# Performance work log

Measured on AMD Instinct MI355X. Metric: run time of the kernel, lower is better.

The kernel has to match this reference:

```python
import jax, jax.numpy as jnp
import numpy as np

B, S, D, H = 8, 2048, 1024, 64


def setup_inputs() -> dict:
    key = jax.random.key(0)
    ks = jax.random.split(key, 9)
    s = 0.02
    return {
        "x": jax.random.normal(ks[0], (B, S, D), jnp.float32),
        "Wq": jax.random.normal(ks[1], (H, D), jnp.float32) * s,
        "bq": jnp.zeros((H,), jnp.float32),
        "Wk": jax.random.normal(ks[2], (H, D), jnp.float32) * s,
        "bk": jnp.zeros((H,), jnp.float32),
        "Wv": jax.random.normal(ks[3], (H, D), jnp.float32) * s,
        "bv": jnp.zeros((H,), jnp.float32),
        "Wo": jax.random.normal(ks[4], (H, H), jnp.float32) * s,
        "bo": jnp.zeros((H,), jnp.float32),
    }


def reference(x, Wq, bq, Wk, bk, Wv, bv, Wo, bo):
    # Linear layers: y = x @ W.T + b (torch nn.Linear convention)
    q = jnp.einsum("bsd,hd->bsh", x, Wq) + bq  # [B,S,H]
    k = jnp.einsum("bsd,hd->bsh", x, Wk) + bk
    v = jnp.einsum("bsd,hd->bsh", x, Wv) + bv
    scale = jnp.float32(H) ** 0.5
    scores = jnp.einsum("bsh,bth->bst", q, k) / scale  # [B,S,S]
    causal = jnp.tril(jnp.ones((S, S), bool))
    scores = jnp.where(causal, scores, -jnp.inf)
    attn = jax.nn.softmax(scores, axis=-1)
    out = jnp.einsum("bst,bth->bsh", attn, v)  # [B,S,H]
    out = jnp.einsum("bsh,gh->bsg", out, Wo) + bo  # output proj [H,H]
    return out
```

## Files before the change

kernel.cpp:

```cpp
#include <hip/hip_runtime.h>
#include <hip/hip_bf16.h>

#define NB 8
#define NS 2048
#define ND 1024
#define NH 64
#define NM (NB*NS)

typedef __attribute__((ext_vector_type(8))) short short8;
typedef __attribute__((ext_vector_type(4))) short short4v;
typedef __attribute__((ext_vector_type(4))) float f32x4;
typedef __attribute__((ext_vector_type(4))) float f4;

#define QSCALE (0.125f * 1.44269504088896340736f)

__device__ __forceinline__ unsigned short f2bf(float f) {
    union { __hip_bfloat16 h; unsigned short u; } cv;
    cv.h = __float2bfloat16(f);
    return cv.u;
}

__global__ __launch_bounds__(256) void convw_kernel(
    const float* __restrict__ Wq, const float* __restrict__ bq,
    const float* __restrict__ Wk, const float* __restrict__ bk,
    const float* __restrict__ Wv, const float* __restrict__ bv,
    const float* __restrict__ Wo,
    unsigned short* __restrict__ Wb, unsigned short* __restrict__ Wob,
    float* __restrict__ biasb)
{
    const int row = blockIdx.x;
    const int t = threadIdx.x;
    if (row < 192) {
        const float* W = row < 64 ? Wq : (row < 128 ? Wk : Wv);
        const float sc = row < 64 ? QSCALE : 1.0f;
        f4 v = *(const f4*)&W[(size_t)(row & 63) * ND + t * 4];
        short4v o;
#pragma unroll
        for (int j = 0; j < 4; ++j) o[j] = (short)f2bf(v[j] * sc);
        *(short4v*)&Wb[(size_t)row * ND + t * 4] = o;
        if (row == 0 && t < 192) {
            const float* bsrc = t < 64 ? bq : (t < 128 ? bk : bv);
            biasb[t] = bsrc[t & 63] * (t < 64 ? QSCALE : 1.0f);
        }
    } else if (t < 16) {
        f4 v = *(const f4*)&Wo[(size_t)(row - 192) * 64 + t * 4];
        short4v o;
#pragma unroll
        for (int j = 0; j < 4; ++j) o[j] = (short)f2bf(v[j]);
        *(short4v*)&Wob[(size_t)(row - 192) * 64 + t * 4] = o;
    }
}

__global__ __launch_bounds__(512) void qkv_kernel(
    const float* __restrict__ x, const unsigned short* __restrict__ Wb,
    const float* __restrict__ biasb,
    unsigned short* __restrict__ q, unsigned short* __restrict__ k,
    unsigned short* __restrict__ vT)
{
    __shared__ unsigned short As[2][64 * 64];
    __shared__ unsigned short Bs[2][192 * 64];

    const int t = threadIdx.x;
    const int lane = t & 63, g = lane >> 4, li = lane & 15;
    const int w = t >> 6, rg = w >> 2, cg = w & 3;
    const int m0 = blockIdx.x * 64;
    const int arow = t >> 3, ach = t & 7;

    f32x4 acc[2][3];
#pragma unroll
    for (int a = 0; a < 2; ++a)
#pragma unroll
        for (int nf = 0; nf < 3; ++nf) acc[a][nf] = (f32x4)0.f;

    f4 xa[2][2]; short8 wr[2][3];

#define QKV_LOAD(KS, SL)                                                          \
    {                                                                             \
        const float* p_ = &x[(size_t)(m0 + arow) * ND + (KS) * 64 + ach * 8];     \
        xa[SL][0] = *(const f4*)p_; xa[SL][1] = *(const f4*)(p_ + 4);             \
        wr[SL][0] = *(const short8*)&Wb[(size_t)(t >> 3) * ND + (KS) * 64 + (t & 7) * 8];                  \
        wr[SL][1] = *(const short8*)&Wb[(size_t)((t + 512) >> 3) * ND + (KS) * 64 + ((t + 512) & 7) * 8];  \
        wr[SL][2] = *(const short8*)&Wb[(size_t)((t + 1024) >> 3) * ND + (KS) * 64 + ((t + 1024) & 7) * 8];\
    }

#define QKV_COMMIT(SL, BUF)                                                       \
    {                                                                             \
        short8 av_;                                                               \
        for (int j_ = 0; j_ < 4; ++j_) {                                          \
            av_[j_] = (short)f2bf(xa[SL][0][j_]);                                 \
            av_[j_ + 4] = (short)f2bf(xa[SL][1][j_]);                             \
        }                                                                         \
        *(short8*)&As[BUF][arow * 64 + ((ach ^ (arow & 7)) << 3)] = av_;          \
        int r0_ = t >> 3, c0_ = t & 7;                                            \
        *(short8*)&Bs[BUF][r0_ * 64 + ((c0_ ^ (r0_ & 7)) << 3)] = wr[SL][0];      \
        int r1_ = (t + 512) >> 3, c1_ = (t + 512) & 7;                            \
        *(short8*)&Bs[BUF][r1_ * 64 + ((c1_ ^ (r1_ & 7)) << 3)] = wr[SL][1];      \
        int r2_ = (t + 1024) >> 3, c2_ = (t + 1024) & 7;                          \
        *(short8*)&Bs[BUF][r2_ * 64 + ((c2_ ^ (r2_ & 7)) << 3)] = wr[SL][2];      \
    }

    QKV_LOAD(0, 0);
    QKV_LOAD(1, 1);
    QKV_COMMIT(0, 0);
    __syncthreads();

#pragma unroll
    for (int ks = 0; ks < 16; ++ks) {
        const int cur = ks & 1;
        if (ks < 14) QKV_LOAD(ks + 2, cur);
#pragma unroll
        for (int h = 0; h < 2; ++h) {
            short8 af0 = *(const short8*)&As[cur][(rg * 32 + 0 + li) * 64 + (((g + 4 * h) ^ (li & 7)) << 3)];
            short8 af1 = *(const short8*)&As[cur][(rg * 32 + 16 + li) * 64 + (((g + 4 * h) ^ (li & 7)) << 3)];
#pragma unroll
            for (int nf = 0; nf < 3; ++nf) {
                short8 bf = *(const short8*)&Bs[cur][(cg * 48 + nf * 16 + li) * 64 + (((g + 4 * h) ^ (li & 7)) << 3)];
                acc[0][nf] = __builtin_amdgcn_mfma_f32_16x16x32_bf16(af0, bf, acc[0][nf], 0, 0, 0);
                acc[1][nf] = __builtin_amdgcn_mfma_f32_16x16x32_bf16(af1, bf, acc[1][nf], 0, 0, 0);
            }
        }
        if (ks < 15) QKV_COMMIT((ks + 1) & 1, cur ^ 1);
        __syncthreads();
    }

#pragma unroll
    for (int nf = 0; nf < 3; ++nf) {
        const int col = cg * 48 + nf * 16 + li;
        const float bias = biasb[col];
#pragma unroll
        for (int a = 0; a < 2; ++a) {
            const int row0 = m0 + rg * 32 + a * 16 + 4 * g;
            if (col < 64) {
#pragma unroll
                for (int i = 0; i < 4; ++i)
                    q[(size_t)(row0 + i) * NH + col] = f2bf(acc[a][nf][i] + bias);
            } else if (col < 128) {
#pragma unroll
                for (int i = 0; i < 4; ++i)
                    k[(size_t)(row0 + i) * NH + (col - 64)] = f2bf(acc[a][nf][i] + bias);
            } else {
                short4v pk;
#pragma unroll
                for (int i = 0; i < 4; ++i) pk[i] = (short)f2bf(acc[a][nf][i] + bias);
                const int bb = row0 >> 11, s = row0 & 2047;
                *(short4v*)&vT[(size_t)(bb * NH + (col - 128)) * NS + s] = pk;
            }
        }
    }
}

__global__ __launch_bounds__(256) void attn_kernel(
    const unsigned short* __restrict__ q, const unsigned short* __restrict__ k,
    const unsigned short* __restrict__ vT,
    float* __restrict__ Opart, float* __restrict__ lpart,
    int ctLog, int MAXC)
{
    __shared__ unsigned short Ks[2][64 * 64];
    __shared__ unsigned short Vs[2][64 * 64];
    __shared__ unsigned short Ps[4][16 * 64];

    const int t = threadIdx.x;
    const int w = t >> 6, lane = t & 63, g = lane >> 4, li = lane & 15;
    const int b = blockIdx.x & 7;
    const int pid = blockIdx.x >> 3;
    const int CT = 1 << ctLog;

    int qt = 0, c = 0;
    {
        int acc = 0;
        for (int u = 31; u >= 0; --u) {
            int nch = (u + CT) >> ctLog;
            if (pid < acc + nch) { qt = u; c = pid - acc; break; }
            acc += nch;
        }
    }
    const int t0 = c * CT;
    const int rem = qt + 1 - t0;
    const int tcount = rem < CT ? rem : CT;

    const size_t qkbase = (size_t)b * NS * NH;
    const int qrow = qt * 64 + w * 16 + li;
    const short8 qa0 = *(const short8*)&q[qkbase + (size_t)qrow * NH + g * 8];
    const short8 qa1 = *(const short8*)&q[qkbase + (size_t)qrow * NH + 32 + g * 8];

    float l_i[4]; f32x4 oacc[4];
#pragma unroll
    for (int i = 0; i < 4; ++i) { l_i[i] = 0.f; oacc[i] = (f32x4)0.f; }

    const int srow = t >> 3, sch = t & 7;
    short8 kreg0, kreg1, vreg0, vreg1;

    {
        const int kv0 = t0 * 64;
        kreg0 = *(const short8*)&k[qkbase + (size_t)(kv0 + srow) * NH + sch * 8];
        kreg1 = *(const short8*)&k[qkbase + (size_t)(kv0 + srow + 32) * NH + sch * 8];
        vreg0 = *(const short8*)&vT[(size_t)(b * NH + srow) * NS + kv0 + sch * 8];
        vreg1 = *(const short8*)&vT[(size_t)(b * NH + srow + 32) * NS + kv0 + sch * 8];
        *(short8*)&Ks[0][srow * 64 + ((sch ^ (srow & 7)) << 3)] = kreg0;
        *(short8*)&Ks[0][(srow + 32) * 64 + ((sch ^ (srow & 7)) << 3)] = kreg1;
        *(short8*)&Vs[0][srow * 64 + ((sch ^ (srow & 7)) << 3)] = vreg0;
        *(short8*)&Vs[0][(srow + 32) * 64 + ((sch ^ (srow & 7)) << 3)] = vreg1;
    }
    __syncthreads();

    for (int tt = 0; tt < tcount; ++tt) {
        const int cur = tt & 1;
        const int kv0 = (t0 + tt) * 64;
        if (tt + 1 < tcount) {
            const int nv0 = kv0 + 64;
            kreg0 = *(const short8*)&k[qkbase + (size_t)(nv0 + srow) * NH + sch * 8];
            kreg1 = *(const short8*)&k[qkbase + (size_t)(nv0 + srow + 32) * NH + sch * 8];
            vreg0 = *(const short8*)&vT[(size_t)(b * NH + srow) * NS + nv0 + sch * 8];
            vreg1 = *(const short8*)&vT[(size_t)(b * NH + srow + 32) * NS + nv0 + sch * 8];
        }
        f32x4 s[4];
#pragma unroll
        for (int c4 = 0; c4 < 4; ++c4) {
            s[c4] = (f32x4)0.f;
            const int krow = 16 * c4 + li;
            short8 kf0 = *(const short8*)&Ks[cur][krow * 64 + ((g ^ (li & 7)) << 3)];
            s[c4] = __builtin_amdgcn_mfma_f32_16x16x32_bf16(qa0, kf0, s[c4], 0, 0, 0);
            short8 kf1 = *(const short8*)&Ks[cur][krow * 64 + (((g + 4) ^ (li & 7)) << 3)];
            s[c4] = __builtin_amdgcn_mfma_f32_16x16x32_bf16(qa1, kf1, s[c4], 0, 0, 0);
        }
        if (kv0 == qt * 64) {
#pragma unroll
            for (int c4 = 0; c4 < 4; ++c4)
#pragma unroll
                for (int i = 0; i < 4; ++i)
                    if (16 * c4 + li > w * 16 + 4 * g + i) s[c4][i] = -1e30f;
        }
        float p[4][4];
#pragma unroll
        for (int c4 = 0; c4 < 4; ++c4)
#pragma unroll
            for (int i = 0; i < 4; ++i)
                p[c4][i] = exp2f(fminf(s[c4][i], 80.f));
#pragma unroll
        for (int i = 0; i < 4; ++i)
            l_i[i] += (p[0][i] + p[1][i]) + (p[2][i] + p[3][i]);

#pragma unroll
        for (int c4 = 0; c4 < 4; ++c4)
#pragma unroll
            for (int i = 0; i < 4; ++i) {
                const int prow = 4 * g + i;
                const int chunk = 2 * c4 + (li >> 3);
                Ps[w][prow * 64 + ((chunk ^ (prow & 7)) << 3) + (li & 7)] = f2bf(p[c4][i]);
            }
        short8 pf0 = *(const short8*)&Ps[w][li * 64 + ((g ^ (li & 7)) << 3)];
        short8 pf1 = *(const short8*)&Ps[w][li * 64 + (((g + 4) ^ (li & 7)) << 3)];
#pragma unroll
        for (int nf = 0; nf < 4; ++nf) {
            const int vrow = nf * 16 + li;
            short8 vf0 = *(const short8*)&Vs[cur][vrow * 64 + ((g ^ (li & 7)) << 3)];
            short8 vf1 = *(const short8*)&Vs[cur][vrow * 64 + (((g + 4) ^ (li & 7)) << 3)];
            oacc[nf] = __builtin_amdgcn_mfma_f32_16x16x32_bf16(pf0, vf0, oacc[nf], 0, 0, 0);
            oacc[nf] = __builtin_amdgcn_mfma_f32_16x16x32_bf16(pf1, vf1, oacc[nf], 0, 0, 0);
        }
        if (tt + 1 < tcount) {
            *(short8*)&Ks[cur ^ 1][srow * 64 + ((sch ^ (srow & 7)) << 3)] = kreg0;
            *(short8*)&Ks[cur ^ 1][(srow + 32) * 64 + ((sch ^ (srow & 7)) << 3)] = kreg1;
            *(short8*)&Vs[cur ^ 1][srow * 64 + ((sch ^ (srow & 7)) << 3)] = vreg0;
            *(short8*)&Vs[cur ^ 1][(srow + 32) * 64 + ((sch ^ (srow & 7)) << 3)] = vreg1;
        }
        __syncthreads();
    }

#pragma unroll
    for (int off = 1; off < 16; off <<= 1)
#pragma unroll
        for (int i = 0; i < 4; ++i) l_i[i] += __shfl_xor(l_i[i], off);

    const size_t slot = (size_t)((b * 32 + qt) * MAXC + c);
    float* Op = Opart + slot * 4096;
#pragma unroll
    for (int nf = 0; nf < 4; ++nf)
#pragma unroll
        for (int i = 0; i < 4; ++i)
            Op[(w * 16 + 4 * g + i) * 64 + nf * 16 + li] = oacc[nf][i];
    if (li == 0) {
#pragma unroll
        for (int i = 0; i < 4; ++i)
            lpart[slot * 64 + w * 16 + 4 * g + i] = l_i[i];
    }
}

__global__ __launch_bounds__(256) void combine_kernel(
    const float* __restrict__ Opart, const float* __restrict__ lpart,
    const unsigned short* __restrict__ Wob, const float* __restrict__ bo,
    float* __restrict__ out, int ctLog, int MAXC)
{
    __shared__ unsigned short Osm[64 * 64];
    __shared__ float Linv[64];

    const int t = threadIdx.x;
    const int b = blockIdx.x & 7, qt = blockIdx.x >> 3;
    const int CT = 1 << ctLog;
    const int nch = (qt + CT) >> ctLog;
    const size_t base_slot = (size_t)(b * 32 + qt) * MAXC;

    if (t < 64) {
        float L = 0.f;
        for (int cc = 0; cc < nch; ++cc)
            L += lpart[(base_slot + cc) * 64 + t];
        Linv[t] = 1.f / L;
    }

    const int r = t >> 2, c0 = (t & 3) * 16;
    f4 a0 = (f4)0.f, a1 = (f4)0.f, a2 = (f4)0.f, a3 = (f4)0.f;
    for (int cc = 0; cc < nch; ++cc) {
        const float* P = Opart + (base_slot + cc) * 4096 + r * 64 + c0;
        a0 += *(const f4*)P; a1 += *(const f4*)(P + 4);
        a2 += *(const f4*)(P + 8); a3 += *(const f4*)(P + 12);
    }
    __syncthreads();
    {
        const float sc = Linv[r];
        short8 o0, o1;
#pragma unroll
        for (int j = 0; j < 4; ++j) {
            o0[j] = (short)f2bf(a0[j] * sc); o0[j + 4] = (short)f2bf(a1[j] * sc);
            o1[j] = (short)f2bf(a2[j] * sc); o1[j + 4] = (short)f2bf(a3[j] * sc);
        }
        const int ch0 = (t & 3) * 2;
        *(short8*)&Osm[r * 64 + ((ch0 ^ (r & 7)) << 3)] = o0;
        *(short8*)&Osm[r * 64 + (((ch0 + 1) ^ (r & 7)) << 3)] = o1;
    }
    __syncthreads();

    const int w = t >> 6, lane = t & 63, g = lane >> 4, li = lane & 15;
    f32x4 acc[4];
#pragma unroll
    for (int nf = 0; nf < 4; ++nf) acc[nf] = (f32x4)0.f;
#pragma unroll
    for (int s = 0; s < 2; ++s) {
        short8 af = *(const short8*)&Osm[(w * 16 + li) * 64 + (((g + 4 * s) ^ (li & 7)) << 3)];
#pragma unroll
        for (int nf = 0; nf < 4; ++nf) {
            short8 bf = *(const short8*)&Wob[(size_t)(nf * 16 + li) * 64 + s * 32 + g * 8];
            acc[nf] = __builtin_amdgcn_mfma_f32_16x16x32_bf16(af, bf, acc[nf], 0, 0, 0);
        }
    }
#pragma unroll
    for (int nf = 0; nf < 4; ++nf) {
        const float bias = bo[nf * 16 + li];
#pragma unroll
        for (int i = 0; i < 4; ++i) {
            const size_t row = (size_t)b * NS + qt * 64 + w * 16 + 4 * g + i;
            out[row * 64 + nf * 16 + li] = acc[nf][i] + bias;
        }
    }
}

extern "C" void kernel_launch(void* const* d_in, const int* in_sizes, int n_in,
                              void* d_out, int out_size, void* d_ws, size_t ws_size,
                              hipStream_t stream)
{
    const float* x  = (const float*)d_in[0];
    const float* Wq = (const float*)d_in[1];
    const float* bq = (const float*)d_in[2];
    const float* Wk = (const float*)d_in[3];
    const float* bk = (const float*)d_in[4];
    const float* Wv = (const float*)d_in[5];
    const float* bv = (const float*)d_in[6];
    const float* Wo = (const float*)d_in[7];
    const float* bo = (const float*)d_in[8];
    float* out = (float*)d_out;

    size_t off = 0;
    auto alloc = [&](size_t bytes) {
        char* p = (char*)d_ws + off;
        off += (bytes + 255) & ~(size_t)255;
        return (void*)p;
    };
    unsigned short* qb  = (unsigned short*)alloc((size_t)NM * NH * 2);
    unsigned short* kb  = (unsigned short*)alloc((size_t)NM * NH * 2);
    unsigned short* vtb = (unsigned short*)alloc((size_t)NM * NH * 2);
    unsigned short* Wb  = (unsigned short*)alloc((size_t)192 * ND * 2);
    unsigned short* Wob = (unsigned short*)alloc((size_t)64 * 64 * 2);
    float* biasb = (float*)alloc(192 * 4);
    const size_t base = off;

    int ctLog = 5, MAXC = 1;
    const int cands[3] = {3, 4, 5};
    for (int ci = 0; ci < 3; ++ci) {
        const int cl = cands[ci];
        const int mc = (31 >> cl) + 1;
        const size_t nslot = (size_t)256 * mc;
        const size_t need = base + nslot * (4096 + 64) * 4 + 8192;
        if (need <= ws_size) { ctLog = cl; MAXC = mc; break; }
    }
    const size_t NSLOT = (size_t)256 * MAXC;
    float* Opart = (float*)alloc(NSLOT * 4096 * 4);
    float* lpart = (float*)alloc(NSLOT * 64 * 4);

    const int CT = 1 << ctLog;
    int NCperB = 0;
    for (int qt = 0; qt < 32; ++qt) NCperB += (qt + CT) >> ctLog;

    convw_kernel<<<256, 256, 0, stream>>>(Wq, bq, Wk, bk, Wv, bv, Wo, Wb, Wob, biasb);
    qkv_kernel<<<NM / 64, 512, 0, stream>>>(x, Wb, biasb, qb, kb, vtb);
    attn_kernel<<<8 * NCperB, 256, 0, stream>>>(qb, kb, vtb, Opart, lpart, ctLog, MAXC);
    combine_kernel<<<256, 256, 0, stream>>>(Opart, lpart, Wob, bo, out, ctLog, MAXC);
}
```

Baseline: 50.21 us.

## Load weights and K/V fragments directly from global into registers, enlarge query tiles

The QKV projection now reads weight fragments straight from global memory into registers with double buffering, dropping the shared-memory B tile and its stores. The attention kernel now processes 128-query blocks, 32 rows per wave, and has each wave load its K and V MFMA fragments directly from global memory with no shared staging or block barriers. Each wave also exits early past the causal boundary. The combine kernel and the workspace slot layout are adjusted to match. This cuts LDS traffic and barrier stalls but adds redundant global/L2 reads across waves and more register pressure.

```diff
diff --git a/kernel.cpp b/kernel.cpp
--- a/kernel.cpp
+++ b/kernel.cpp
@@ -58,7 +58,6 @@
     unsigned short* __restrict__ vT)
 {
     __shared__ unsigned short As[2][64 * 64];
-    __shared__ unsigned short Bs[2][192 * 64];
 
     const int t = threadIdx.x;
     const int lane = t & 63, g = lane >> 4, li = lane & 15;
@@ -72,54 +71,59 @@
 #pragma unroll
         for (int nf = 0; nf < 3; ++nf) acc[a][nf] = (f32x4)0.f;
 
-    f4 xa[2][2]; short8 wr[2][3];
-
-#define QKV_LOAD(KS, SL)                                                          \
-    {                                                                             \
-        const float* p_ = &x[(size_t)(m0 + arow) * ND + (KS) * 64 + ach * 8];     \
-        xa[SL][0] = *(const f4*)p_; xa[SL][1] = *(const f4*)(p_ + 4);             \
-        wr[SL][0] = *(const short8*)&Wb[(size_t)(t >> 3) * ND + (KS) * 64 + (t & 7) * 8];                  \
-        wr[SL][1] = *(const short8*)&Wb[(size_t)((t + 512) >> 3) * ND + (KS) * 64 + ((t + 512) & 7) * 8];  \
-        wr[SL][2] = *(const short8*)&Wb[(size_t)((t + 1024) >> 3) * ND + (KS) * 64 + ((t + 1024) & 7) * 8];\
-    }
-
-#define QKV_COMMIT(SL, BUF)                                                       \
-    {                                                                             \
-        short8 av_;                                                               \
-        for (int j_ = 0; j_ < 4; ++j_) {                                          \
-            av_[j_] = (short)f2bf(xa[SL][0][j_]);                                 \
-            av_[j_ + 4] = (short)f2bf(xa[SL][1][j_]);                             \
-        }                                                                         \
-        *(short8*)&As[BUF][arow * 64 + ((ach ^ (arow & 7)) << 3)] = av_;          \
-        int r0_ = t >> 3, c0_ = t & 7;                                            \
-        *(short8*)&Bs[BUF][r0_ * 64 + ((c0_ ^ (r0_ & 7)) << 3)] = wr[SL][0];      \
-        int r1_ = (t + 512) >> 3, c1_ = (t + 512) & 7;                            \
-        *(short8*)&Bs[BUF][r1_ * 64 + ((c1_ ^ (r1_ & 7)) << 3)] = wr[SL][1];      \
-        int r2_ = (t + 1024) >> 3, c2_ = (t + 1024) & 7;                          \
-        *(short8*)&Bs[BUF][r2_ * 64 + ((c2_ ^ (r2_ & 7)) << 3)] = wr[SL][2];      \
-    }
-
-    QKV_LOAD(0, 0);
-    QKV_LOAD(1, 1);
-    QKV_COMMIT(0, 0);
+    f4 xa[2][2];
+    short8 bfr[2][3][2];
+
+#define XLOAD(KS, SL)                                                         \
+    {                                                                         \
+        const float* p_ = &x[(size_t)(m0 + arow) * ND + (KS) * 64 + ach * 8]; \
+        xa[SL][0] = *(const f4*)p_; xa[SL][1] = *(const f4*)(p_ + 4);         \
+    }
+
+#define XCOMMIT(SL, BUF)                                                      \
+    {                                                                         \
+        short8 av_;                                                           \
+        for (int j_ = 0; j_ < 4; ++j_) {                                      \
+            av_[j_] = (short)f2bf(xa[SL][0][j_]);                             \
+            av_[j_ + 4] = (short)f2bf(xa[SL][1][j_]);                         \
+        }                                                                     \
+        *(short8*)&As[BUF][arow * 64 + ((ach ^ (arow & 7)) << 3)] = av_;      \
+    }
+
+#define WLOAD(KS, SL)                                                         \
+    {                                                                         \
+        _Pragma("unroll")                                                     \
+        for (int nf_ = 0; nf_ < 3; ++nf_)                                     \
+            _Pragma("unroll")                                                 \
+            for (int h_ = 0; h_ < 2; ++h_)                                    \
+                bfr[SL][nf_][h_] = *(const short8*)&Wb[                       \
+                    (size_t)(cg * 48 + nf_ * 16 + li) * ND + (KS) * 64 +      \
+                    h_ * 32 + g * 8];                                         \
+    }
+
+    XLOAD(0, 0);
+    XLOAD(1, 1);
+    WLOAD(0, 0);
+    XCOMMIT(0, 0);
     __syncthreads();
 
 #pragma unroll
     for (int ks = 0; ks < 16; ++ks) {
         const int cur = ks & 1;
-        if (ks < 14) QKV_LOAD(ks + 2, cur);
+        const int wb = ks & 1;
+        if (ks < 15) WLOAD(ks + 1, wb ^ 1);
+        if (ks < 14) XLOAD(ks + 2, cur);
 #pragma unroll
         for (int h = 0; h < 2; ++h) {
             short8 af0 = *(const short8*)&As[cur][(rg * 32 + 0 + li) * 64 + (((g + 4 * h) ^ (li & 7)) << 3)];
             short8 af1 = *(const short8*)&As[cur][(rg * 32 + 16 + li) * 64 + (((g + 4 * h) ^ (li & 7)) << 3)];
 #pragma unroll
             for (int nf = 0; nf < 3; ++nf) {
-                short8 bf = *(const short8*)&Bs[cur][(cg * 48 + nf * 16 + li) * 64 + (((g + 4 * h) ^ (li & 7)) << 3)];
-                acc[0][nf] = __builtin_amdgcn_mfma_f32_16x16x32_bf16(af0, bf, acc[0][nf], 0, 0, 0);
-                acc[1][nf] = __builtin_amdgcn_mfma_f32_16x16x32_bf16(af1, bf, acc[1][nf], 0, 0, 0);
+                acc[0][nf] = __builtin_amdgcn_mfma_f32_16x16x32_bf16(af0, bfr[wb][nf][h], acc[0][nf], 0, 0, 0);
+                acc[1][nf] = __builtin_amdgcn_mfma_f32_16x16x32_bf16(af1, bfr[wb][nf][h], acc[1][nf], 0, 0, 0);
             }
         }
-        if (ks < 15) QKV_COMMIT((ks + 1) & 1, cur ^ 1);
+        if (ks < 15) XCOMMIT((ks + 1) & 1, cur ^ 1);
         __syncthreads();
     }
 
@@ -155,9 +159,7 @@
     float* __restrict__ Opart, float* __restrict__ lpart,
     int ctLog, int MAXC)
 {
-    __shared__ unsigned short Ks[2][64 * 64];
-    __shared__ unsigned short Vs[2][64 * 64];
-    __shared__ unsigned short Ps[4][16 * 64];
+    __shared__ unsigned short Ps[4][32 * 64];
 
     const int t = threadIdx.x;
     const int w = t >> 6, lane = t & 63, g = lane >> 4, li = lane & 15;
@@ -165,124 +167,137 @@
     const int pid = blockIdx.x >> 3;
     const int CT = 1 << ctLog;
 
-    int qt = 0, c = 0;
+    int qb = 0, c = 0;
     {
         int acc = 0;
-        for (int u = 31; u >= 0; --u) {
-            int nch = (u + CT) >> ctLog;
-            if (pid < acc + nch) { qt = u; c = pid - acc; break; }
+        for (int u = 15; u >= 0; --u) {
+            const int nch = (2 * u + 2 + CT - 1) >> ctLog;
+            if (pid < acc + nch) { qb = u; c = pid - acc; break; }
             acc += nch;
         }
     }
     const int t0 = c * CT;
-    const int rem = qt + 1 - t0;
+    const int ntt = 2 * qb + 2;
+    const int rem = ntt - t0;
     const int tcount = rem < CT ? rem : CT;
 
     const size_t qkbase = (size_t)b * NS * NH;
-    const int qrow = qt * 64 + w * 16 + li;
-    const short8 qa0 = *(const short8*)&q[qkbase + (size_t)qrow * NH + g * 8];
-    const short8 qa1 = *(const short8*)&q[qkbase + (size_t)qrow * NH + 32 + g * 8];
-
-    float l_i[4]; f32x4 oacc[4];
-#pragma unroll
-    for (int i = 0; i < 4; ++i) { l_i[i] = 0.f; oacc[i] = (f32x4)0.f; }
-
-    const int srow = t >> 3, sch = t & 7;
-    short8 kreg0, kreg1, vreg0, vreg1;
-
-    {
-        const int kv0 = t0 * 64;
-        kreg0 = *(const short8*)&k[qkbase + (size_t)(kv0 + srow) * NH + sch * 8];
-        kreg1 = *(const short8*)&k[qkbase + (size_t)(kv0 + srow + 32) * NH + sch * 8];
-        vreg0 = *(const short8*)&vT[(size_t)(b * NH + srow) * NS + kv0 + sch * 8];
-        vreg1 = *(const short8*)&vT[(size_t)(b * NH + srow + 32) * NS + kv0 + sch * 8];
-        *(short8*)&Ks[0][srow * 64 + ((sch ^ (srow & 7)) << 3)] = kreg0;
-        *(short8*)&Ks[0][(srow + 32) * 64 + ((sch ^ (srow & 7)) << 3)] = kreg1;
-        *(short8*)&Vs[0][srow * 64 + ((sch ^ (srow & 7)) << 3)] = vreg0;
-        *(short8*)&Vs[0][(srow + 32) * 64 + ((sch ^ (srow & 7)) << 3)] = vreg1;
-    }
-    __syncthreads();
+    const int q0 = qb * 128 + w * 32;
+    const int qmax = q0 + 31;
+
+    short8 qa[2][2];
+#pragma unroll
+    for (int qs = 0; qs < 2; ++qs)
+#pragma unroll
+        for (int h = 0; h < 2; ++h)
+            qa[qs][h] = *(const short8*)&q[qkbase + (size_t)(q0 + qs * 16 + li) * NH + h * 32 + g * 8];
+
+    float l_i[2][4];
+    f32x4 oacc[2][4];
+#pragma unroll
+    for (int qs = 0; qs < 2; ++qs)
+#pragma unroll
+        for (int i = 0; i < 4; ++i) { l_i[qs][i] = 0.f; oacc[qs][i] = (f32x4)0.f; }
 
     for (int tt = 0; tt < tcount; ++tt) {
-        const int cur = tt & 1;
         const int kv0 = (t0 + tt) * 64;
-        if (tt + 1 < tcount) {
-            const int nv0 = kv0 + 64;
-            kreg0 = *(const short8*)&k[qkbase + (size_t)(nv0 + srow) * NH + sch * 8];
-            kreg1 = *(const short8*)&k[qkbase + (size_t)(nv0 + srow + 32) * NH + sch * 8];
-            vreg0 = *(const short8*)&vT[(size_t)(b * NH + srow) * NS + nv0 + sch * 8];
-            vreg1 = *(const short8*)&vT[(size_t)(b * NH + srow + 32) * NS + nv0 + sch * 8];
-        }
-        f32x4 s[4];
-#pragma unroll
-        for (int c4 = 0; c4 < 4; ++c4) {
-            s[c4] = (f32x4)0.f;
-            const int krow = 16 * c4 + li;
-            short8 kf0 = *(const short8*)&Ks[cur][krow * 64 + ((g ^ (li & 7)) << 3)];
-            s[c4] = __builtin_amdgcn_mfma_f32_16x16x32_bf16(qa0, kf0, s[c4], 0, 0, 0);
-            short8 kf1 = *(const short8*)&Ks[cur][krow * 64 + (((g + 4) ^ (li & 7)) << 3)];
-            s[c4] = __builtin_amdgcn_mfma_f32_16x16x32_bf16(qa1, kf1, s[c4], 0, 0, 0);
-        }
-        if (kv0 == qt * 64) {
+        if (kv0 > qmax) break;
+
+        short8 kf[4][2];
+#pragma unroll
+        for (int c4 = 0; c4 < 4; ++c4)
+#pragma unroll
+            for (int h = 0; h < 2; ++h)
+                kf[c4][h] = *(const short8*)&k[qkbase + (size_t)(kv0 + 16 * c4 + li) * NH + h * 32 + g * 8];
+
+        f32x4 s[2][4];
+#pragma unroll
+        for (int qs = 0; qs < 2; ++qs)
+#pragma unroll
+            for (int c4 = 0; c4 < 4; ++c4) {
+                s[qs][c4] = (f32x4)0.f;
+                s[qs][c4] = __builtin_amdgcn_mfma_f32_16x16x32_bf16(qa[qs][0], kf[c4][0], s[qs][c4], 0, 0, 0);
+                s[qs][c4] = __builtin_amdgcn_mfma_f32_16x16x32_bf16(qa[qs][1], kf[c4][1], s[qs][c4], 0, 0, 0);
+            }
+
+        short8 vf[4][2];
+#pragma unroll
+        for (int nf = 0; nf < 4; ++nf)
+#pragma unroll
+            for (int h = 0; h < 2; ++h)
+                vf[nf][h] = *(const short8*)&vT[(size_t)(b * NH + nf * 16 + li) * NS + kv0 + h * 32 + g * 8];
+
+        if (kv0 + 63 > q0) {
+#pragma unroll
+            for (int qs = 0; qs < 2; ++qs)
+#pragma unroll
+                for (int c4 = 0; c4 < 4; ++c4)
+#pragma unroll
+                    for (int i = 0; i < 4; ++i)
+                        if (kv0 + 16 * c4 + li > q0 + qs * 16 + 4 * g + i)
+                            s[qs][c4][i] = -1e30f;
+        }
+
+        float p[2][4][4];
+#pragma unroll
+        for (int qs = 0; qs < 2; ++qs) {
 #pragma unroll
             for (int c4 = 0; c4 < 4; ++c4)
 #pragma unroll
                 for (int i = 0; i < 4; ++i)
-                    if (16 * c4 + li > w * 16 + 4 * g + i) s[c4][i] = -1e30f;
-        }
-        float p[4][4];
-#pragma unroll
-        for (int c4 = 0; c4 < 4; ++c4)
+                    p[qs][c4][i] = exp2f(fminf(s[qs][c4][i], 80.f));
 #pragma unroll
             for (int i = 0; i < 4; ++i)
-                p[c4][i] = exp2f(fminf(s[c4][i], 80.f));
-#pragma unroll
-        for (int i = 0; i < 4; ++i)
-            l_i[i] += (p[0][i] + p[1][i]) + (p[2][i] + p[3][i]);
-
-#pragma unroll
-        for (int c4 = 0; c4 < 4; ++c4)
-#pragma unroll
-            for (int i = 0; i < 4; ++i) {
-                const int prow = 4 * g + i;
-                const int chunk = 2 * c4 + (li >> 3);
-                Ps[w][prow * 64 + ((chunk ^ (prow & 7)) << 3) + (li & 7)] = f2bf(p[c4][i]);
+                l_i[qs][i] += (p[qs][0][i] + p[qs][1][i]) + (p[qs][2][i] + p[qs][3][i]);
+        }
+
+#pragma unroll
+        for (int qs = 0; qs < 2; ++qs)
+#pragma unroll
+            for (int c4 = 0; c4 < 4; ++c4)
+#pragma unroll
+                for (int i = 0; i < 4; ++i) {
+                    const int prow = qs * 16 + 4 * g + i;
+                    const int chunk = 2 * c4 + (li >> 3);
+                    Ps[w][prow * 64 + ((chunk ^ (prow & 7)) << 3) + (li & 7)] = f2bf(p[qs][c4][i]);
+                }
+
+#pragma unroll
+        for (int qs = 0; qs < 2; ++qs) {
+            const int prr = qs * 16 + li;
+            short8 pf0 = *(const short8*)&Ps[w][prr * 64 + ((g ^ (prr & 7)) << 3)];
+            short8 pf1 = *(const short8*)&Ps[w][prr * 64 + (((g + 4) ^ (prr & 7)) << 3)];
+#pragma unroll
+            for (int nf = 0; nf < 4; ++nf) {
+                oacc[qs][nf] = __builtin_amdgcn_mfma_f32_16x16x32_bf16(pf0, vf[nf][0], oacc[qs][nf], 0, 0, 0);
+                oacc[qs][nf] = __builtin_amdgcn_mfma_f32_16x16x32_bf16(pf1, vf[nf][1], oacc[qs][nf], 0, 0, 0);
             }
-        short8 pf0 = *(const short8*)&Ps[w][li * 64 + ((g ^ (li & 7)) << 3)];
-        short8 pf1 = *(const short8*)&Ps[w][li * 64 + (((g + 4) ^ (li & 7)) << 3)];
-#pragma unroll
-        for (int nf = 0; nf < 4; ++nf) {
-            const int vrow = nf * 16 + li;
-            short8 vf0 = *(const short8*)&Vs[cur][vrow * 64 + ((g ^ (li & 7)) << 3)];
-            short8 vf1 = *(const short8*)&Vs[cur][vrow * 64 + (((g + 4) ^ (li & 7)) << 3)];
-            oacc[nf] = __builtin_amdgcn_mfma_f32_16x16x32_bf16(pf0, vf0, oacc[nf], 0, 0, 0);
-            oacc[nf] = __builtin_amdgcn_mfma_f32_16x16x32_bf16(pf1, vf1, oacc[nf], 0, 0, 0);
-        }
-        if (tt + 1 < tcount) {
-            *(short8*)&Ks[cur ^ 1][srow * 64 + ((sch ^ (srow & 7)) << 3)] = kreg0;
-            *(short8*)&Ks[cur ^ 1][(srow + 32) * 64 + ((sch ^ (srow & 7)) << 3)] = kreg1;
-            *(short8*)&Vs[cur ^ 1][srow * 64 + ((sch ^ (srow & 7)) << 3)] = vreg0;
-            *(short8*)&Vs[cur ^ 1][(srow + 32) * 64 + ((sch ^ (srow & 7)) << 3)] = vreg1;
-        }
-        __syncthreads();
+        }
     }
 
 #pragma unroll
     for (int off = 1; off < 16; off <<= 1)
 #pragma unroll
-        for (int i = 0; i < 4; ++i) l_i[i] += __shfl_xor(l_i[i], off);
-
-    const size_t slot = (size_t)((b * 32 + qt) * MAXC + c);
-    float* Op = Opart + slot * 4096;
-#pragma unroll
-    for (int nf = 0; nf < 4; ++nf)
-#pragma unroll
-        for (int i = 0; i < 4; ++i)
-            Op[(w * 16 + 4 * g + i) * 64 + nf * 16 + li] = oacc[nf][i];
+        for (int qs = 0; qs < 2; ++qs)
+#pragma unroll
+            for (int i = 0; i < 4; ++i)
+                l_i[qs][i] += __shfl_xor(l_i[qs][i], off);
+
+    const size_t slot = (size_t)((b * 16 + qb) * MAXC + c);
+    float* Op = Opart + slot * 8192;
+#pragma unroll
+    for (int qs = 0; qs < 2; ++qs)
+#pragma unroll
+        for (int nf = 0; nf < 4; ++nf)
+#pragma unroll
+            for (int i = 0; i < 4; ++i)
+                Op[(w * 32 + qs * 16 + 4 * g + i) * 64 + nf * 16 + li] = oacc[qs][nf][i];
     if (li == 0) {
 #pragma unroll
-        for (int i = 0; i < 4; ++i)
-            lpart[slot * 64 + w * 16 + 4 * g + i] = l_i[i];
+        for (int qs = 0; qs < 2; ++qs)
+#pragma unroll
+            for (int i = 0; i < 4; ++i)
+                lpart[slot * 128 + w * 32 + qs * 16 + 4 * g + i] = l_i[qs][i];
     }
 }
 
@@ -295,22 +310,23 @@
     __shared__ float Linv[64];
 
     const int t = threadIdx.x;
-    const int b = blockIdx.x & 7, qt = blockIdx.x >> 3;
+    const int b = blockIdx.x & 7, qb = (blockIdx.x >> 3) & 15, half = blockIdx.x >> 7;
+    const int r0 = half * 64;
     const int CT = 1 << ctLog;
-    const int nch = (qt + CT) >> ctLog;
-    const size_t base_slot = (size_t)(b * 32 + qt) * MAXC;
+    const int nch = (2 * qb + 2 + CT - 1) >> ctLog;
+    const size_t base_slot = (size_t)(b * 16 + qb) * MAXC;
 
     if (t < 64) {
         float L = 0.f;
         for (int cc = 0; cc < nch; ++cc)
-            L += lpart[(base_slot + cc) * 64 + t];
+            L += lpart[(base_slot + cc) * 128 + r0 + t];
         Linv[t] = 1.f / L;
     }
 
     const int r = t >> 2, c0 = (t & 3) * 16;
     f4 a0 = (f4)0.f, a1 = (f4)0.f, a2 = (f4)0.f, a3 = (f4)0.f;
     for (int cc = 0; cc < nch; ++cc) {
-        const float* P = Opart + (base_slot + cc) * 4096 + r * 64 + c0;
+        const float* P = Opart + (base_slot + cc) * 8192 + (r0 + r) * 64 + c0;
         a0 += *(const f4*)P; a1 += *(const f4*)(P + 4);
         a2 += *(const f4*)(P + 8); a3 += *(const f4*)(P + 12);
     }
@@ -347,7 +363,7 @@
         const float bias = bo[nf * 16 + li];
 #pragma unroll
         for (int i = 0; i < 4; ++i) {
-            const size_t row = (size_t)b * NS + qt * 64 + w * 16 + 4 * g + i;
+            const size_t row = (size_t)b * NS + qb * 128 + r0 + w * 16 + 4 * g + i;
             out[row * 64 + nf * 16 + li] = acc[nf][i] + bias;
         }
     }
@@ -383,21 +399,21 @@
     const size_t base = off;
 
     int ctLog = 5, MAXC = 1;
-    const int cands[3] = {3, 4, 5};
-    for (int ci = 0; ci < 3; ++ci) {
+    const int cands[4] = {2, 3, 4, 5};
+    for (int ci = 0; ci < 4; ++ci) {
         const int cl = cands[ci];
-        const int mc = (31 >> cl) + 1;
-        const size_t nslot = (size_t)256 * mc;
-        const size_t need = base + nslot * (4096 + 64) * 4 + 8192;
+        const int mc = 32 >> cl;
+        const size_t nslot = (size_t)128 * mc;
+        const size_t need = base + nslot * (8192 + 128) * 4 + 8192;
         if (need <= ws_size) { ctLog = cl; MAXC = mc; break; }
     }
-    const size_t NSLOT = (size_t)256 * MAXC;
-    float* Opart = (float*)alloc(NSLOT * 4096 * 4);
-    float* lpart = (float*)alloc(NSLOT * 64 * 4);
+    const size_t NSLOT = (size_t)128 * MAXC;
+    float* Opart = (float*)alloc(NSLOT * 8192 * 4);
+    float* lpart = (float*)alloc(NSLOT * 128 * 4);
 
     const int CT = 1 << ctLog;
     int NCperB = 0;
-    for (int qt = 0; qt < 32; ++qt) NCperB += (qt + CT) >> ctLog;
+    for (int qt = 0; qt < 16; ++qt) NCperB += (2 * qt + 2 + CT - 1) >> ctLog;
 
     convw_kernel<<<256, 256, 0, stream>>>(Wq, bq, Wk, bk, Wv, bv, Wo, Wb, Wob, biasb);
     qkv_kernel<<<NM / 64, 512, 0, stream>>>(x, Wb, biasb, qb, kb, vtb);
```

After: 74.26 us. 1.48x slower.
